# Performance work log

Hardware: AMD Instinct MI355X
Metric: run time of the kernel (lower is better)

Reference implementation:

```python
import jax, jax.numpy as jnp
import numpy as np

D_MODEL = 1024; D_STATE = 64; D_CONV = 4; EXPAND = 2; HEADDIM = 128; NGROUPS = 1; CHUNK = 256
D_INNER = EXPAND * D_MODEL            # 2048
NHEADS = D_INNER // HEADDIM           # 16
CONV_DIM = D_INNER + 2 * NGROUPS * D_STATE   # 2176
D_IN_PROJ = 2 * D_INNER + 2 * NGROUPS * D_STATE + NHEADS  # 4240
B = 4; G = 256; L = 2048
EPS = 1e-5


def setup_inputs() -> dict:
    key = jax.random.key(0)
    ks = jax.random.split(key, 12)
    def nrm(k, shape, s=0.02):
        return jax.random.normal(k, shape, jnp.float32) * s
    return dict(
        local_repr=jax.random.normal(ks[0], (B, L, D_MODEL), jnp.float32),
        global_repr=jax.random.normal(ks[1], (B, G, D_MODEL), jnp.float32),
        norm1_w=jnp.ones((D_MODEL,), jnp.float32), norm1_b=jnp.zeros((D_MODEL,), jnp.float32),
        norm2_w=jnp.ones((D_MODEL,), jnp.float32), norm2_b=jnp.zeros((D_MODEL,), jnp.float32),
        norm3_w=jnp.ones((D_MODEL,), jnp.float32), norm3_b=jnp.zeros((D_MODEL,), jnp.float32),
        in_proj_w=nrm(ks[2], (D_IN_PROJ, D_MODEL)),
        conv_w=nrm(ks[3], (CONV_DIM, D_CONV), 0.2),
        conv_b=jnp.zeros((CONV_DIM,), jnp.float32),
        dt_bias=jnp.log(jnp.expm1(jax.random.uniform(ks[4], (NHEADS,), jnp.float32, 1e-3, 0.1))),
        A_log=jnp.log(jax.random.uniform(ks[5], (NHEADS,), jnp.float32, 1.0, 16.0)),
        D_skip=jnp.ones((NHEADS,), jnp.float32),
        ssd_norm_w=jnp.ones((D_INNER,), jnp.float32),
        out_proj_w=nrm(ks[6], (D_MODEL, D_INNER)),
        ffn_w1=nrm(ks[7], (D_MODEL // 2, D_MODEL)),
        ffn_b1=jnp.zeros((D_MODEL // 2,), jnp.float32),
        ffn_w2=nrm(ks[8], (D_MODEL, D_MODEL // 2)),
        ffn_b2=jnp.zeros((D_MODEL,), jnp.float32),
    )


def _ln(x, w, b):
    mu = jnp.mean(x, axis=-1, keepdims=True)
    var = jnp.mean((x - mu) ** 2, axis=-1, keepdims=True)
    return (x - mu) * jax.lax.rsqrt(var + EPS) * w + b


def _segsum(a):
    # a: (..., T) -> (..., T, T) lower-triangular sums a[j+1..i]
    T = a.shape[-1]
    cs = jnp.cumsum(a, axis=-1)
    diff = cs[..., :, None] - cs[..., None, :]
    mask = jnp.tril(jnp.ones((T, T), bool))
    return jnp.where(mask, diff, -jnp.inf)


def _ssd(xdt, a_dt, Bh, Ch):
    # xdt: (b,t,h,p) = x*dt ; a_dt: (b,t,h) = dt*A ; Bh,Ch: (b,t,h,n)
    b, t, h, p = xdt.shape
    n = Bh.shape[-1]
    c = t // CHUNK
    X = xdt.reshape(b, c, CHUNK, h, p)
    Bc = Bh.reshape(b, c, CHUNK, h, n)
    Cc = Ch.reshape(b, c, CHUNK, h, n)
    Ac = a_dt.reshape(b, c, CHUNK, h).transpose(0, 3, 1, 2)  # (b,h,c,k)
    A_cum = jnp.cumsum(Ac, axis=-1)
    Lm = jnp.exp(_segsum(Ac))                                # (b,h,c,k,k)
    Y_diag = jnp.einsum('bckhn,bcshn,bhcks,bcshp->bckhp', Cc, Bc, Lm, X)
    decay_states = jnp.exp(A_cum[..., -1:] - A_cum)          # (b,h,c,k)
    states = jnp.einsum('bckhn,bhck,bckhp->bchpn', Bc, decay_states, X)
    A_last = jnp.pad(A_cum[..., -1], ((0, 0), (0, 0), (1, 0)))
    decay_chunk = jnp.exp(_segsum(A_last))                   # (b,h,c+1,c+1)
    states = jnp.concatenate([jnp.zeros_like(states[:, :1]), states], axis=1)
    new_states = jnp.einsum('bhzc,bchpn->bzhpn', decay_chunk, states)
    states_in = new_states[:, :-1]                           # (b,c,h,p,n)
    out_decay = jnp.exp(A_cum)                               # (b,h,c,k)
    Y_off = jnp.einsum('bckhn,bchpn,bhck->bckhp', Cc, states_in, out_decay)
    return (Y_diag + Y_off).reshape(b, t, h, p)


def _mamba2(x, in_proj_w, conv_w, conv_b, dt_bias, A_log, D_skip, ssd_norm_w, out_proj_w):
    b, t, _ = x.shape
    zxbcdt = x @ in_proj_w.T                                  # (b,t,D_IN_PROJ)
    z = zxbcdt[..., :D_INNER]
    xBC = zxbcdt[..., D_INNER:D_INNER + CONV_DIM]
    dt = jax.nn.softplus(zxbcdt[..., D_INNER + CONV_DIM:] + dt_bias)  # (b,t,h)
    # causal depthwise conv1d, kernel D_CONV
    xp = jnp.pad(xBC, ((0, 0), (D_CONV - 1, 0), (0, 0)))
    xBC = sum(xp[:, i:i + t, :] * conv_w[:, i] for i in range(D_CONV)) + conv_b
    xBC = jax.nn.silu(xBC)
    xs = xBC[..., :D_INNER].reshape(b, t, NHEADS, HEADDIM)
    Bm = xBC[..., D_INNER:D_INNER + NGROUPS * D_STATE].reshape(b, t, NGROUPS, D_STATE)
    Cm = xBC[..., D_INNER + NGROUPS * D_STATE:].reshape(b, t, NGROUPS, D_STATE)
    rep = NHEADS // NGROUPS
    Bh = jnp.repeat(Bm, rep, axis=2)
    Ch = jnp.repeat(Cm, rep, axis=2)
    A = -jnp.exp(A_log)                                       # (h,)
    Y = _ssd(xs * dt[..., None], dt * A, Bh, Ch)
    y = Y + D_skip[None, None, :, None] * xs
    y = y.reshape(b, t, D_INNER)
    # gated RMSNorm (norm_before_gate=False)
    y = y * jax.nn.silu(z)
    y = y * jax.lax.rsqrt(jnp.mean(y * y, axis=-1, keepdims=True) + EPS) * ssd_norm_w
    return y @ out_proj_w.T


def reference(local_repr, global_repr, norm1_w, norm1_b, norm2_w, norm2_b, norm3_w, norm3_b,
              in_proj_w, conv_w, conv_b, dt_bias, A_log, D_skip, ssd_norm_w, out_proj_w,
              ffn_w1, ffn_b1, ffn_w2, ffn_b2):
    local_n = _ln(local_repr, norm1_w, norm1_b)
    global_n = _ln(global_repr, norm2_w, norm2_b)
    x = jnp.concatenate([global_n, local_n], axis=1)          # (B, G+L, D)
    x = _mamba2(x, in_proj_w, conv_w, conv_b, dt_bias, A_log, D_skip, ssd_norm_w, out_proj_w)
    x = x[:, -local_n.shape[1]:, :] + local_n
    x = _ln(x, norm3_w, norm3_b)
    h = jax.nn.gelu(x @ ffn_w1.T + ffn_b1, approximate=False)
    return (h @ ffn_w2.T + ffn_b2) + x
```

## Files before the change

kernel.cpp:

```cpp
#include <hip/hip_runtime.h>
#include <math.h>

#define B_ 4
#define L_ 2048
#define G_ 256
#define T_ 2304
#define DM 1024
#define DINNER 2048
#define NH 16
#define HD 128
#define NSTATE 64
#define CONVD 2176
#define DPROJ 4240
#define NPROJ_PAD 4352
#define NCHUNK 9
#define CK 256
#define EPSV 1e-5f
#define CROWS 16

typedef unsigned short bf16t;
using bf16x8 = __attribute__((ext_vector_type(8))) short;
using f32x4  = __attribute__((ext_vector_type(4))) float;

__device__ __forceinline__ float bf2f(bf16t u) {
  return __uint_as_float(((unsigned int)u) << 16);
}
__device__ __forceinline__ bf16t f2bf(float f) {
  unsigned int u = __float_as_uint(f);
  u += 0x7FFFu + ((u >> 16) & 1u);
  return (bf16t)(u >> 16);
}

__device__ __forceinline__ void g2lds16(const bf16t* g, short* l) {
  __builtin_amdgcn_global_load_lds(
      (const __attribute__((address_space(1))) unsigned int*)g,
      (__attribute__((address_space(3))) unsigned int*)l, 16, 0, 0);
}

__device__ __forceinline__ float2 block_reduce2(float a, float b) {
  __shared__ float sa[4], sb[4];
  #pragma unroll
  for (int off = 32; off > 0; off >>= 1) {
    a += __shfl_down(a, off, 64);
    b += __shfl_down(b, off, 64);
  }
  int lane = threadIdx.x & 63, wid = threadIdx.x >> 6;
  if (lane == 0) { sa[wid] = a; sb[wid] = b; }
  __syncthreads();
  return make_float2(sa[0] + sa[1] + sa[2] + sa[3], sb[0] + sb[1] + sb[2] + sb[3]);
}

__global__ __launch_bounds__(256) void ln_cvt_kernel(
    const float* __restrict__ localr, const float* __restrict__ globalr,
    const float* __restrict__ w1, const float* __restrict__ b1,
    const float* __restrict__ w2, const float* __restrict__ b2,
    bf16t* __restrict__ x, const float* __restrict__ inpw,
    bf16t* __restrict__ inpw_bf) {
  int blk = blockIdx.x;
  if (blk < B_ * T_) {
    int t = blk % T_, b = blk / T_;
    const float *src, *w, *bb;
    if (t < G_) { src = globalr + ((long)b * G_ + t) * DM;        w = w2; bb = b2; }
    else        { src = localr  + ((long)b * L_ + (t - G_)) * DM; w = w1; bb = b1; }
    int d = threadIdx.x * 4;
    float4 v = *(const float4*)&src[d];
    float s = v.x + v.y + v.z + v.w;
    float sq = v.x * v.x + v.y * v.y + v.z * v.z + v.w * v.w;
    float2 r2 = block_reduce2(s, sq);
    float mu = r2.x * (1.f / DM);
    float var = r2.y * (1.f / DM) - mu * mu;
    float rstd = rsqrtf(var + EPSV);
    float4 wv = *(const float4*)&w[d];
    float4 bv = *(const float4*)&bb[d];
    ushort4 o;
    o.x = f2bf((v.x - mu) * rstd * wv.x + bv.x);
    o.y = f2bf((v.y - mu) * rstd * wv.y + bv.y);
    o.z = f2bf((v.z - mu) * rstd * wv.z + bv.z);
    o.w = f2bf((v.w - mu) * rstd * wv.w + bv.w);
    *(ushort4*)&x[(long)blk * DM + d] = o;
  } else {
    long i = (long)(blk - B_ * T_) * 1024 + threadIdx.x * 4;
    const long nreal = (long)DPROJ * DM, ntot = (long)NPROJ_PAD * DM;
    if (i < ntot) {
      ushort4 o = {0, 0, 0, 0};
      if (i < nreal) {
        float4 v = *(const float4*)&inpw[i];
        o.x = f2bf(v.x); o.y = f2bf(v.y); o.z = f2bf(v.z); o.w = f2bf(v.w);
      }
      *(ushort4*)&inpw_bf[i] = o;
    }
  }
}

__global__ __launch_bounds__(512, 2) void gemm_inproj(
    const bf16t* __restrict__ A, const bf16t* __restrict__ W,
    bf16t* __restrict__ z, bf16t* __restrict__ xpre, float* __restrict__ dtr) {
  __shared__ short LDS8[65536];
  int tid = threadIdx.x;
  int lane = tid & 63, w = tid >> 6;
  int wm = w >> 2, wn = w & 3;
  int l15 = lane & 15;
  int bn = blockIdx.x * 256, bm = blockIdx.y * 256;

  int csub = ((lane & 7) ^ (lane >> 3)) * 8;
  const bf16t* srcA = A + (long)(bm + w * 16 + (lane >> 3)) * 1024 + csub;
  const bf16t* srcW = W + (long)(bn + w * 16 + (lane >> 3)) * 1024 + csub;
  int stageDst = w * 1024 + lane * 8;

  int aoff0 = l15 * 64 + (((lane >> 4) + 0) ^ (lane & 7)) * 8;
  int aoff1 = l15 * 64 + (((lane >> 4) + 4) ^ (lane & 7)) * 8;
  int boff0 = ((wn & 1) * 64 + l15) * 64 + (((lane >> 4) + 0) ^ (lane & 7)) * 8;
  int boff1 = ((wn & 1) * 64 + l15) * 64 + (((lane >> 4) + 4) ^ (lane & 7)) * 8;
  int aBase0 = wm * 8192;
  int bBase0 = 16384 + (wn >> 1) * 8192;

  f32x4 acc[8][4] = {};
  bf16x8 af[4][2], bq[4][2];

#define STAGE2(gsrc, ldsoff) do { \
    g2lds16((gsrc), LDS8 + (ldsoff) + stageDst); \
    g2lds16((gsrc) + 8 * 1024, LDS8 + (ldsoff) + stageDst + 512); } while (0)

  STAGE2(srcA, 0);
  STAGE2(srcA + 128 * 1024, 8192);
  STAGE2(srcW, 16384);
  STAGE2(srcW + 128 * 1024, 24576);
  STAGE2(srcW + 64, 32768 + 16384);
  STAGE2(srcW + 128 * 1024 + 64, 32768 + 24576);
  asm volatile("s_waitcnt vmcnt(4)" ::: "memory");
  __builtin_amdgcn_s_barrier();

  const int nt = 16;
  #pragma unroll 2
  for (int t = 0; t < nt; ++t) {
    int cs_ = (t & 1) * 32768;
    int ns_ = 32768 - cs_;
    const short* aB = LDS8 + cs_ + aBase0;
    const short* bB = LDS8 + cs_ + bBase0;

    #pragma unroll
    for (int mi = 0; mi < 4; mi++) {
      af[mi][0] = *(const bf16x8*)&aB[mi * 1024 + aoff0];
      af[mi][1] = *(const bf16x8*)&aB[mi * 1024 + aoff1];
    }
    #pragma unroll
    for (int ni = 0; ni < 2; ni++) {
      bq[ni][0] = *(const bf16x8*)&bB[ni * 1024 + boff0];
      bq[ni][1] = *(const bf16x8*)&bB[ni * 1024 + boff1];
    }
    if (t + 1 < nt) STAGE2(srcA + (t + 1) * 64, ns_);
    __builtin_amdgcn_s_barrier();
    __builtin_amdgcn_s_setprio(1);
    #pragma unroll
    for (int ks = 0; ks < 2; ks++)
      #pragma unroll
      for (int mi = 0; mi < 4; mi++)
        #pragma unroll
        for (int ni = 0; ni < 2; ni++)
          acc[mi][ni] = __builtin_amdgcn_mfma_f32_16x16x32_bf16(af[mi][ks], bq[ni][ks], acc[mi][ni], 0, 0, 0);
    __builtin_amdgcn_s_setprio(0);
    __builtin_amdgcn_s_barrier();

    #pragma unroll
    for (int ni = 2; ni < 4; ni++) {
      bq[ni][0] = *(const bf16x8*)&bB[ni * 1024 + boff0];
      bq[ni][1] = *(const bf16x8*)&bB[ni * 1024 + boff1];
    }
    if (t + 1 < nt) STAGE2(srcA + 128 * 1024 + (t + 1) * 64, ns_ + 8192);
    __builtin_amdgcn_s_barrier();
    __builtin_amdgcn_s_setprio(1);
    #pragma unroll
    for (int ks = 0; ks < 2; ks++)
      #pragma unroll
      for (int mi = 0; mi < 4; mi++)
        #pragma unroll
        for (int ni = 2; ni < 4; ni++)
          acc[mi][ni] = __builtin_amdgcn_mfma_f32_16x16x32_bf16(af[mi][ks], bq[ni][ks], acc[mi][ni], 0, 0, 0);
    __builtin_amdgcn_s_setprio(0);
    __builtin_amdgcn_s_barrier();

    #pragma unroll
    for (int mi = 0; mi < 4; mi++) {
      af[mi][0] = *(const bf16x8*)&aB[(mi + 4) * 1024 + aoff0];
      af[mi][1] = *(const bf16x8*)&aB[(mi + 4) * 1024 + aoff1];
    }
    if (t + 2 < nt) STAGE2(srcW + (t + 2) * 64, cs_ + 16384);
    __builtin_amdgcn_s_barrier();
    __builtin_amdgcn_s_setprio(1);
    #pragma unroll
    for (int ks = 0; ks < 2; ks++)
      #pragma unroll
      for (int mi = 0; mi < 4; mi++)
        #pragma unroll
        for (int ni = 2; ni < 4; ni++)
          acc[mi + 4][ni] = __builtin_amdgcn_mfma_f32_16x16x32_bf16(af[mi][ks], bq[ni][ks], acc[mi + 4][ni], 0, 0, 0);
    __builtin_amdgcn_s_setprio(0);
    __builtin_amdgcn_s_barrier();

    if (t + 2 < nt) STAGE2(srcW + 128 * 1024 + (t + 2) * 64, cs_ + 24576);
    __builtin_amdgcn_s_barrier();
    __builtin_amdgcn_s_setprio(1);
    #pragma unroll
    for (int ks = 0; ks < 2; ks++)
      #pragma unroll
      for (int mi = 0; mi < 4; mi++)
        #pragma unroll
        for (int ni = 0; ni < 2; ni++)
          acc[mi + 4][ni] = __builtin_amdgcn_mfma_f32_16x16x32_bf16(af[mi][ks], bq[ni][ks], acc[mi + 4][ni], 0, 0, 0);
    __builtin_amdgcn_s_setprio(0);
    if (t + 2 < nt)      asm volatile("s_waitcnt vmcnt(4)" ::: "memory");
    else if (t + 1 < nt) asm volatile("s_waitcnt vmcnt(0)" ::: "memory");
    __builtin_amdgcn_s_barrier();
  }
#undef STAGE2

  if (bn == 4096 && wn == 2) {
    #pragma unroll
    for (int mi = 0; mi < 8; mi++)
      #pragma unroll
      for (int r = 0; r < 4; r++) {
        int row = bm + wm * 128 + mi * 16 + (lane >> 4) * 4 + r;
        dtr[(long)row * NH + l15] = acc[mi][0][r];
      }
  }

  bf16t* Cs = (bf16t*)LDS8;
  #pragma unroll
  for (int pass = 0; pass < 2; pass++) {
    __syncthreads();
    if (wm == pass) {
      #pragma unroll
      for (int mi = 0; mi < 8; mi++)
        #pragma unroll
        for (int ni = 0; ni < 4; ni++)
          #pragma unroll
          for (int r = 0; r < 4; r++)
            Cs[(mi * 16 + (lane >> 4) * 4 + r) * 264 + wn * 64 + ni * 16 + l15] =
                f2bf(acc[mi][ni][r]);
    }
    __syncthreads();
    #pragma unroll
    for (int q = 0; q < 8; q++) {
      int idx = q * 512 + tid;
      int row = idx >> 5, cg = idx & 31;
      int gcol = bn + cg * 8;
      long grow = bm + pass * 128 + row;
      if (gcol < DINNER + CONVD) {
        bf16x8 v = *(bf16x8*)&Cs[row * 264 + cg * 8];
        if (gcol < DINNER) *(bf16x8*)&z[grow * DINNER + gcol] = v;
        else               *(bf16x8*)&xpre[grow * CONVD + (gcol - DINNER)] = v;
      }
    }
  }
}

template<int EPI, bool OFFS>
__global__ __launch_bounds__(256) void gemm_mfma(
    const bf16t* __restrict__ A, const bf16t* __restrict__ W,
    const float* __restrict__ bias, const bf16t* __restrict__ res,
    float* __restrict__ Cf, bf16t* __restrict__ Cb,
    bf16t* __restrict__ z, bf16t* __restrict__ xpre, float* __restrict__ dtr,
    int N, int K) {
  __shared__ __align__(16) short LDS[128 * 136];
  short* As = LDS;
  short* Ws = LDS + 128 * 32;
  int tid = threadIdx.x;
  int lane = tid & 63, w = tid >> 6;
  int wr = w >> 1, wc = w & 1;
  int bm = blockIdx.y * 128, bn = blockIdx.x * 128;
  long bmA = OFFS ? ((long)(bm >> 11) * T_ + G_ + (bm & 2047)) : (long)bm;

  int r1 = tid >> 2,         s1 = (((tid & 3) ^ ((r1 >> 1) & 3))) * 8;
  int r2 = (tid + 256) >> 2, s2 = (((tid & 3) ^ ((r2 >> 1) & 3))) * 8;
  const bf16t* gA1 = A + (bmA + r1) * K + s1;
  const bf16t* gA2 = A + (bmA + r2) * K + s2;
  const bf16t* gW1 = W + (long)(bn + r1) * K + s1;
  const bf16t* gW2 = W + (long)(bn + r2) * K + s2;
  short* lA1 = As + tid * 8;
  short* lA2 = As + (tid + 256) * 8;
  short* lW1 = Ws + tid * 8;
  short* lW2 = Ws + (tid + 256) * 8;

  int arow = wr * 64 + (lane & 15);
  int brow = wc * 64 + (lane & 15);
  int koff = (((lane >> 4) ^ (((lane & 15) >> 1) & 3))) * 8;

  f32x4 acc[4][4] = {};
  for (int k0 = 0; k0 < K; k0 += 32) {
    g2lds16(gA1 + k0, lA1);
    g2lds16(gA2 + k0, lA2);
    g2lds16(gW1 + k0, lW1);
    g2lds16(gW2 + k0, lW2);
    __syncthreads();
    bf16x8 af[4], bf[4];
    #pragma unroll
    for (int mi = 0; mi < 4; mi++) af[mi] = *(bf16x8*)&As[(arow + mi * 16) * 32 + koff];
    #pragma unroll
    for (int ni = 0; ni < 4; ni++) bf[ni] = *(bf16x8*)&Ws[(brow + ni * 16) * 32 + koff];
    #pragma unroll
    for (int mi = 0; mi < 4; mi++)
      #pragma unroll
      for (int ni = 0; ni < 4; ni++)
        acc[mi][ni] = __builtin_amdgcn_mfma_f32_16x16x32_bf16(af[mi], bf[ni], acc[mi][ni], 0, 0, 0);
    __syncthreads();
  }

  int rb = wr * 64 + (lane >> 4) * 4;
  int cb = wc * 64 + (lane & 15);

  if (EPI == 3) {
    float* Cs32 = (float*)LDS;
    #pragma unroll
    for (int pass = 0; pass < 2; pass++) {
      __syncthreads();
      if (wr == pass) {
        #pragma unroll
        for (int mi = 0; mi < 4; mi++)
          #pragma unroll
          for (int ni = 0; ni < 4; ni++)
            #pragma unroll
            for (int r = 0; r < 4; r++) {
              int lrow = (lane >> 4) * 4 + mi * 16 + r;
              Cs32[lrow * 136 + cb + ni * 16] = acc[mi][ni][r];
            }
      }
      __syncthreads();
      #pragma unroll
      for (int q = 0; q < 4; q++) {
        int row = q * 16 + (tid >> 4);
        int col = (tid & 15) * 8;
        long grow = bm + pass * 64 + row; int gcol = bn + col;
        float4 v0 = *(float4*)&Cs32[row * 136 + col];
        float4 v1 = *(float4*)&Cs32[row * 136 + col + 4];
        float4 b0 = *(const float4*)&bias[gcol];
        float4 b1 = *(const float4*)&bias[gcol + 4];
        bf16x8 rv = *(const bf16x8*)&res[grow * N + gcol];
        v0.x += b0.x + bf2f((bf16t)rv[0]); v0.y += b0.y + bf2f((bf16t)rv[1]);
        v0.z += b0.z + bf2f((bf16t)rv[2]); v0.w += b0.w + bf2f((bf16t)rv[3]);
        v1.x += b1.x + bf2f((bf16t)rv[4]); v1.y += b1.y + bf2f((bf16t)rv[5]);
        v1.z += b1.z + bf2f((bf16t)rv[6]); v1.w += b1.w + bf2f((bf16t)rv[7]);
        *(float4*)&Cf[grow * N + gcol] = v0;
        *(float4*)&Cf[grow * N + gcol + 4] = v1;
      }
    }
    return;
  }

  __syncthreads();
  bf16t* Cs = (bf16t*)LDS;
  #pragma unroll
  for (int mi = 0; mi < 4; mi++)
    #pragma unroll
    for (int ni = 0; ni < 4; ni++)
      #pragma unroll
      for (int r = 0; r < 4; r++) {
        float v = acc[mi][ni][r];
        if (EPI == 2) {
          v += bias[bn + cb + ni * 16];
          v = 0.5f * v * (1.f + erff(v * 0.70710678118f));
        }
        Cs[(rb + mi * 16 + r) * 136 + cb + ni * 16] = f2bf(v);
      }
  __syncthreads();
  #pragma unroll
  for (int pass = 0; pass < 8; pass++) {
    int row = pass * 16 + (tid >> 4);
    int col = (tid & 15) * 8;
    bf16x8 vv = *(bf16x8*)&Cs[row * 136 + col];
    long grow = bm + row; int gcol = bn + col;
    *(bf16x8*)&Cb[grow * N + gcol] = vv;
  }
}

__global__ __launch_bounds__(256) void cumsum_kernel(
    const float* __restrict__ dtraw, const float* __restrict__ dt_bias,
    const float* __restrict__ A_log, float* __restrict__ dt,
    float* __restrict__ Acum) {
  int bid = blockIdx.x;
  int c = bid % NCHUNK; int hh = bid / NCHUNK;
  int h = hh % NH; int b = hh / NH;
  int k = threadIdx.x;
  float a = -__expf(A_log[h]);
  long t = (long)b * T_ + c * CK + k;
  float v0 = dtraw[t * NH + h] + dt_bias[h];
  float dtv = (v0 > 20.f) ? v0 : log1pf(__expf(v0));
  dt[t * NH + h] = dtv;
  float v = dtv * a;
  __shared__ float buf[2][CK];
  int cur = 0;
  buf[0][k] = v; __syncthreads();
  for (int off = 1; off < CK; off <<= 1) {
    float tv = buf[cur][k];
    if (k >= off) tv += buf[cur][k - off];
    buf[1 - cur][k] = tv; cur ^= 1; __syncthreads();
  }
  Acum[(long)bid * CK + k] = buf[cur][k];
}

__global__ __launch_bounds__(256) void conv_kernel(
    const bf16t* __restrict__ xpre, const float* __restrict__ cw,
    const float* __restrict__ cb, bf16t* __restrict__ out) {
  int gt = blockIdx.x * 256 + threadIdx.x;
  int cg = gt % 272; int rt = gt / 272;
  int c0 = cg * 8;
  long r0 = (long)rt * CROWS;
  int t0 = (int)(r0 % T_);

  float wreg[4][8];
  #pragma unroll
  for (int j = 0; j < 8; j++) {
    float4 wa = *(const float4*)&cw[(c0 + j) * 4];
    wreg[0][j] = wa.x; wreg[1][j] = wa.y; wreg[2][j] = wa.z; wreg[3][j] = wa.w;
  }
  float4 cb0 = *(const float4*)&cb[c0];
  float4 cb1 = *(const float4*)&cb[c0 + 4];
  float bias[8] = {cb0.x, cb0.y, cb0.z, cb0.w, cb1.x, cb1.y, cb1.z, cb1.w};

  bf16x8 win[4];
  #pragma unroll
  for (int i = 0; i < 3; i++) {
    if (t0 - 3 + i >= 0) win[i] = *(const bf16x8*)&xpre[(r0 - 3 + i) * CONVD + c0];
    else                 win[i] = bf16x8{0,0,0,0,0,0,0,0};
  }

  #pragma unroll
  for (int k = 0; k < CROWS; k++) {
    win[3] = *(const bf16x8*)&xpre[(r0 + k) * CONVD + c0];
    float acc[8];
    #pragma unroll
    for (int j = 0; j < 8; j++) acc[j] = bias[j];
    #pragma unroll
    for (int i = 0; i < 4; i++)
      #pragma unroll
      for (int j = 0; j < 8; j++)
        acc[j] += bf2f((bf16t)win[i][j]) * wreg[i][j];
    bf16x8 o;
    #pragma unroll
    for (int j = 0; j < 8; j++) {
      float s = acc[j] / (1.f + __expf(-acc[j]));
      o[j] = (short)f2bf(s);
    }
    *(bf16x8*)&out[(r0 + k) * CONVD + c0] = o;
    win[0] = win[1]; win[1] = win[2]; win[2] = win[3];
  }
}

__global__ __launch_bounds__(256) void chunk_states_kernel(
    const bf16t* __restrict__ xbc, const float* __restrict__ dt,
    const float* __restrict__ Acum, float* __restrict__ cs) {
  int bid = blockIdx.x;
  int h = bid & 15; int bc = bid >> 4;
  int c = bc & 7; int b = bc >> 3;
  int tid = threadIdx.x;
  int lane = tid & 63, w = tid >> 6;
  long tch = (long)b * T_ + c * CK;
  int acb = ((b * NH + h) * NCHUNK + c) * CK;
  float Alast = Acum[acb + CK - 1];

  __shared__ bf16t Xt[128][72];
  __shared__ bf16t Bt[64][72];
  __shared__ float wk[64];

  f32x4 acc[8] = {};
  for (int kb = 0; kb < 4; kb++) {
    int s0 = kb * 64;
    __syncthreads();
    if (tid < 64)
      wk[tid] = __expf(Alast - Acum[acb + s0 + tid]) * dt[(tch + s0 + tid) * NH + h];
    __syncthreads();
    for (int e = tid; e < 64 * 32; e += 256) {
      int s = e & 63, p4 = e >> 6;
      ushort4 u = *(const ushort4*)&xbc[(tch + s0 + s) * CONVD + h * HD + p4 * 4];
      float wv = wk[s];
      Xt[p4 * 4 + 0][s] = f2bf(bf2f(u.x) * wv);
      Xt[p4 * 4 + 1][s] = f2bf(bf2f(u.y) * wv);
      Xt[p4 * 4 + 2][s] = f2bf(bf2f(u.z) * wv);
      Xt[p4 * 4 + 3][s] = f2bf(bf2f(u.w) * wv);
    }
    for (int e = tid; e < 64 * 16; e += 256) {
      int s = e & 63, n4 = e >> 6;
      ushort4 u = *(const ushort4*)&xbc[(tch + s0 + s) * CONVD + DINNER + n4 * 4];
      Bt[n4 * 4 + 0][s] = u.x; Bt[n4 * 4 + 1][s] = u.y;
      Bt[n4 * 4 + 2][s] = u.z; Bt[n4 * 4 + 3][s] = u.w;
    }
    __syncthreads();
    #pragma unroll
    for (int ks = 0; ks < 2; ks++) {
      int koff = (lane >> 4) * 8 + ks * 32;
      bf16x8 bfr = *(bf16x8*)&Bt[w * 16 + (lane & 15)][koff];
      #pragma unroll
      for (int mi = 0; mi < 8; mi++) {
        bf16x8 af = *(bf16x8*)&Xt[mi * 16 + (lane & 15)][koff];
        acc[mi] = __builtin_amdgcn_mfma_f32_16x16x32_bf16(af, bfr, acc[mi], 0, 0, 0);
      }
    }
  }
  int cbid = (b * NCHUNK + c) * NH + h;
  float* out = cs + (long)cbid * HD * NSTATE;
  int n = w * 16 + (lane & 15);
  #pragma unroll
  for (int mi = 0; mi < 8; mi++) {
    #pragma unroll
    for (int r = 0; r < 4; r++) {
      int p = mi * 16 + (lane >> 4) * 4 + r;
      out[p * NSTATE + n] = acc[mi][r];
    }
  }
}

__global__ __launch_bounds__(256) void state_pass_kernel(
    float* __restrict__ cs, const float* __restrict__ Acum) {
  int bh = blockIdx.x;
  int b = bh / NH, h = bh % NH;
  int e0 = blockIdx.y * 1024 + threadIdx.x;
  for (int q = 0; q < 4; q++) {
    int e = e0 + q * 256;
    float s = 0.f;
    for (int c = 0; c < NCHUNK; c++) {
      long idx = ((long)(b * NCHUNK + c) * NH + h) * (HD * NSTATE) + e;
      if (c < NCHUNK - 1) {
        float tmp = cs[idx];
        cs[idx] = s;
        float g = __expf(Acum[((b * NH + h) * NCHUNK + c) * CK + CK - 1]);
        s = s * g + tmp;
      } else {
        cs[idx] = s;
      }
    }
  }
}

__global__ __launch_bounds__(256) void ssd_y_kernel(
    const bf16t* __restrict__ xbc, const float* __restrict__ dt,
    const float* __restrict__ Acum, const float* __restrict__ sin_,
    const float* __restrict__ Dskip, bf16t* __restrict__ Y) {
  int bid = blockIdx.x;
  int h = bid & 15; int bc = bid >> 4;
  int c = 1 + (bc & 7); int b = bc >> 3;
  int rt = blockIdx.y;
  int tid = threadIdx.x;
  int lane = tid & 63, w = tid >> 6;
  int wr = w >> 1, wc = w & 1;
  long tch = (long)b * T_ + c * CK;
  long tbase = tch + rt * 128;
  int acb = ((b * NH + h) * NCHUNK + c) * CK;

  __shared__ bf16t Cs[128][72];
  __shared__ bf16t Bs[64][72];
  __shared__ bf16t Xt[128][72];
  __shared__ bf16t Sm[128][72];
  __shared__ float Akl[128];
  __shared__ float Asl[64];
  __shared__ float dts[64];

  for (int e = tid; e < 128 * 8; e += 256) {
    int row = e >> 3, seg = (e & 7) * 8;
    *(bf16x8*)&Cs[row][seg] =
        *(const bf16x8*)&xbc[(tbase + row) * CONVD + DINNER + NSTATE + seg];
  }
  if (tid < 128) Akl[tid] = Acum[acb + rt * 128 + tid];

  f32x4 acc[4][4] = {};
  int nsb = 2 * (rt + 1);
  for (int sb = 0; sb < nsb; sb++) {
    int s0 = sb * 64;
    __syncthreads();
    if (tid < 64) {
      Asl[tid] = Acum[acb + s0 + tid];
      dts[tid] = dt[(tch + s0 + tid) * NH + h];
    }
    __syncthreads();
    for (int e = tid; e < 64 * 8; e += 256) {
      int row = e >> 3, seg = (e & 7) * 8;
      *(bf16x8*)&Bs[row][seg] =
          *(const bf16x8*)&xbc[(tch + s0 + row) * CONVD + DINNER + seg];
    }
    for (int e = tid; e < 64 * 32; e += 256) {
      int s = e & 63, p4 = e >> 6;
      ushort4 u = *(const ushort4*)&xbc[(tch + s0 + s) * CONVD + h * HD + p4 * 4];
      float dtv = dts[s];
      Xt[p4 * 4 + 0][s] = f2bf(bf2f(u.x) * dtv);
      Xt[p4 * 4 + 1][s] = f2bf(bf2f(u.y) * dtv);
      Xt[p4 * 4 + 2][s] = f2bf(bf2f(u.z) * dtv);
      Xt[p4 * 4 + 3][s] = f2bf(bf2f(u.w) * dtv);
    }
    __syncthreads();
    {
      f32x4 sacc[2][4] = {};
      int rw0 = w * 32;
      #pragma unroll
      for (int ks = 0; ks < 2; ks++) {
        int koff = (lane >> 4) * 8 + ks * 32;
        bf16x8 a0 = *(bf16x8*)&Cs[rw0 + (lane & 15)][koff];
        bf16x8 a1 = *(bf16x8*)&Cs[rw0 + 16 + (lane & 15)][koff];
        #pragma unroll
        for (int ni = 0; ni < 4; ni++) {
          bf16x8 bfr = *(bf16x8*)&Bs[ni * 16 + (lane & 15)][koff];
          sacc[0][ni] = __builtin_amdgcn_mfma_f32_16x16x32_bf16(a0, bfr, sacc[0][ni], 0, 0, 0);
          sacc[1][ni] = __builtin_amdgcn_mfma_f32_16x16x32_bf16(a1, bfr, sacc[1][ni], 0, 0, 0);
        }
      }
      #pragma unroll
      for (int mi = 0; mi < 2; mi++) {
        #pragma unroll
        for (int ni = 0; ni < 4; ni++) {
          #pragma unroll
          for (int r = 0; r < 4; r++) {
            int row = rw0 + mi * 16 + (lane >> 4) * 4 + r;
            int scol = ni * 16 + (lane & 15);
            int kglob = rt * 128 + row;
            int sglob = s0 + scol;
            float val = 0.f;
            if (sglob <= kglob) val = sacc[mi][ni][r] * __expf(Akl[row] - Asl[scol]);
            Sm[row][scol] = f2bf(val);
          }
        }
      }
    }
    __syncthreads();
    #pragma unroll
    for (int ks = 0; ks < 2; ks++) {
      int koff = (lane >> 4) * 8 + ks * 32;
      bf16x8 af[4], bfr[4];
      #pragma unroll
      for (int mi = 0; mi < 4; mi++) af[mi] = *(bf16x8*)&Sm[wr * 64 + mi * 16 + (lane & 15)][koff];
      #pragma unroll
      for (int ni = 0; ni < 4; ni++) bfr[ni] = *(bf16x8*)&Xt[wc * 64 + ni * 16 + (lane & 15)][koff];
      #pragma unroll
      for (int mi = 0; mi < 4; mi++)
        #pragma unroll
        for (int ni = 0; ni < 4; ni++)
          acc[mi][ni] = __builtin_amdgcn_mfma_f32_16x16x32_bf16(af[mi], bfr[ni], acc[mi][ni], 0, 0, 0);
    }
  }

  float ekr[16];
  #pragma unroll
  for (int mi = 0; mi < 4; mi++)
    #pragma unroll
    for (int r = 0; r < 4; r++)
      ekr[mi * 4 + r] = __expf(Akl[wr * 64 + mi * 16 + (lane >> 4) * 4 + r]);

  int cbid = (b * NCHUNK + c) * NH + h;
  const float* sinb = sin_ + (long)cbid * HD * NSTATE;
  #pragma unroll
  for (int ni = 0; ni < 4; ni++) {
    f32x4 offacc[4] = {};
    int p = wc * 64 + ni * 16 + (lane & 15);
    #pragma unroll
    for (int ks = 0; ks < 2; ks++) {
      int koff = (lane >> 4) * 8 + ks * 32;
      const float* srow = sinb + p * NSTATE + koff;
      float4 sa = *(const float4*)srow;
      float4 sbv = *(const float4*)(srow + 4);
      bf16x8 bfr;
      bfr[0] = (short)f2bf(sa.x);  bfr[1] = (short)f2bf(sa.y);
      bfr[2] = (short)f2bf(sa.z);  bfr[3] = (short)f2bf(sa.w);
      bfr[4] = (short)f2bf(sbv.x); bfr[5] = (short)f2bf(sbv.y);
      bfr[6] = (short)f2bf(sbv.z); bfr[7] = (short)f2bf(sbv.w);
      #pragma unroll
      for (int mi = 0; mi < 4; mi++) {
        bf16x8 af = *(bf16x8*)&Cs[wr * 64 + mi * 16 + (lane & 15)][koff];
        offacc[mi] = __builtin_amdgcn_mfma_f32_16x16x32_bf16(af, bfr, offacc[mi], 0, 0, 0);
      }
    }
    #pragma unroll
    for (int mi = 0; mi < 4; mi++)
      #pragma unroll
      for (int r = 0; r < 4; r++)
        acc[mi][ni][r] += ekr[mi * 4 + r] * offacc[mi][r];
  }

  float dsk = Dskip[h];
  #pragma unroll
  for (int mi = 0; mi < 4; mi++) {
    #pragma unroll
    for (int r = 0; r < 4; r++) {
      int row = wr * 64 + mi * 16 + (lane >> 4) * 4 + r;
      long t = tbase + row;
      #pragma unroll
      for (int ni = 0; ni < 4; ni++) {
        int p = wc * 64 + ni * 16 + (lane & 15);
        float xsv = bf2f(xbc[t * CONVD + h * HD + p]);
        Y[t * DINNER + h * HD + p] = f2bf(acc[mi][ni][r] + dsk * xsv);
      }
    }
  }
}

__global__ __launch_bounds__(256) void gate_rms_cvt_kernel(
    const bf16t* __restrict__ z, const float* __restrict__ nw,
    bf16t* __restrict__ Y,
    const float* __restrict__ outw, const float* __restrict__ f1w,
    const float* __restrict__ f2w, bf16t* __restrict__ o_out,
    bf16t* __restrict__ o_f1, bf16t* __restrict__ o_f2) {
  int blk = blockIdx.x;
  if (blk < B_ * L_) {
    long r = (long)(blk >> 11) * T_ + G_ + (blk & 2047);
    const bf16t* zrow = z + r * DINNER;
    bf16t* yrow = Y + r * DINNER;
    int tid = threadIdx.x;
    float v[8]; float sq = 0.f;
    #pragma unroll
    for (int i = 0; i < 4; i++) {
      int d = tid * 2 + 512 * i;
      ushort2 zu = *(const ushort2*)&zrow[d];
      ushort2 yu = *(const ushort2*)&yrow[d];
      float z0 = bf2f(zu.x), z1 = bf2f(zu.y);
      float y0 = bf2f(yu.x) * (z0 / (1.f + __expf(-z0)));
      float y1 = bf2f(yu.y) * (z1 / (1.f + __expf(-z1)));
      v[2 * i] = y0; v[2 * i + 1] = y1;
      sq += y0 * y0 + y1 * y1;
    }
    float2 r2 = block_reduce2(sq, 0.f);
    float rms = rsqrtf(r2.x * (1.f / DINNER) + EPSV);
    #pragma unroll
    for (int i = 0; i < 4; i++) {
      int d = tid * 2 + 512 * i;
      ushort2 o;
      o.x = f2bf(v[2 * i] * rms * nw[d]);
      o.y = f2bf(v[2 * i + 1] * rms * nw[d + 1]);
      *(ushort2*)&yrow[d] = o;
    }
  } else {
    long i = (long)(blk - B_ * L_) * 1024 + threadIdx.x * 4;
    const long n1 = (long)DM * DINNER;
    const long n2 = (long)(DM / 2) * DM;
    const float* src; bf16t* dst; long off;
    if (i < n1) { src = outw; dst = o_out; off = i; }
    else if (i < n1 + n2) { src = f1w; dst = o_f1; off = i - n1; }
    else { src = f2w; dst = o_f2; off = i - n1 - n2; }
    float4 v = *(const float4*)&src[off];
    ushort4 o;
    o.x = f2bf(v.x); o.y = f2bf(v.y); o.z = f2bf(v.z); o.w = f2bf(v.w);
    *(ushort4*)&dst[off] = o;
  }
}

__global__ __launch_bounds__(256) void res_ln3_kernel(
    const bf16t* __restrict__ mfull, const bf16t* __restrict__ x,
    const float* __restrict__ w3, const float* __restrict__ b3,
    bf16t* __restrict__ x2) {
  int rl = blockIdx.x;
  int tl = rl & 2047, b = rl >> 11;
  long rt = (long)b * T_ + G_ + tl;
  const bf16t* m = mfull + (long)rl * DM;
  const bf16t* xr = x + rt * DM;
  int tid = threadIdx.x;
  float v[4]; float s = 0.f, sq = 0.f;
  #pragma unroll
  for (int i = 0; i < 2; i++) {
    int d = tid * 2 + 512 * i;
    ushort2 mu2 = *(const ushort2*)&m[d];
    ushort2 xu2 = *(const ushort2*)&xr[d];
    float a0 = bf2f(mu2.x) + bf2f(xu2.x);
    float a1 = bf2f(mu2.y) + bf2f(xu2.y);
    v[2 * i] = a0; v[2 * i + 1] = a1;
    s += a0 + a1; sq += a0 * a0 + a1 * a1;
  }
  float2 r2 = block_reduce2(s, sq);
  float mu = r2.x * (1.f / DM);
  float var = r2.y * (1.f / DM) - mu * mu;
  float rstd = rsqrtf(var + EPSV);
  bf16t* dst = x2 + (long)rl * DM;
  #pragma unroll
  for (int i = 0; i < 2; i++) {
    int d = tid * 2 + 512 * i;
    ushort2 o;
    o.x = f2bf((v[2 * i] - mu) * rstd * w3[d] + b3[d]);
    o.y = f2bf((v[2 * i + 1] - mu) * rstd * w3[d + 1] + b3[d + 1]);
    *(ushort2*)&dst[d] = o;
  }
}

extern "C" void kernel_launch(void* const* d_in, const int* in_sizes, int n_in,
                              void* d_out, int out_size, void* d_ws, size_t ws_size,
                              hipStream_t stream) {
  const float* localr = (const float*)d_in[0];
  const float* globalr= (const float*)d_in[1];
  const float* n1w = (const float*)d_in[2];
  const float* n1b = (const float*)d_in[3];
  const float* n2w = (const float*)d_in[4];
  const float* n2b = (const float*)d_in[5];
  const float* n3w = (const float*)d_in[6];
  const float* n3b = (const float*)d_in[7];
  const float* inpw= (const float*)d_in[8];
  const float* convw=(const float*)d_in[9];
  const float* convb=(const float*)d_in[10];
  const float* dtb = (const float*)d_in[11];
  const float* alog= (const float*)d_in[12];
  const float* dskp= (const float*)d_in[13];
  const float* ssdw= (const float*)d_in[14];
  const float* outw= (const float*)d_in[15];
  const float* f1w = (const float*)d_in[16];
  const float* f1b = (const float*)d_in[17];
  const float* f2w = (const float*)d_in[18];
  const float* f2b = (const float*)d_in[19];

  char* ws = (char*)d_ws;
  bf16t* x     = (bf16t*)(ws + 0);
  bf16t* z     = (bf16t*)(ws + 18874368);
  bf16t* mfull = (bf16t*)(ws + 18874368);
  bf16t* xpre  = (bf16t*)(ws + 56623104);
  bf16t* Yb    = (bf16t*)(ws + 56623104);
  float* dtraw = (float*)(ws + 96731136);
  float* dt    = (float*)(ws + 97320960);
  float* Acum  = (float*)(ws + 97910784);
  bf16t* xbc   = (bf16t*)(ws + 98500608);
  bf16t* x2bf  = (bf16t*)(ws + 98500608);
  bf16t* hbuf  = (bf16t*)(ws + 115277824);
  bf16t* outw_bf = (bf16t*)(ws + 123666432);
  bf16t* f1w_bf  = (bf16t*)(ws + 127860736);
  bf16t* f2w_bf  = (bf16t*)(ws + 128909312);
  float* cs    = (float*)(ws + 138608640);
  bf16t* inpw_bf = (bf16t*)(ws + 138608640);

  ln_cvt_kernel<<<B_ * T_ + 4352, 256, 0, stream>>>(
      localr, globalr, n1w, n1b, n2w, n2b, x, inpw, inpw_bf);

  gemm_inproj<<<dim3(NPROJ_PAD / 256, (B_ * T_) / 256), 512, 0, stream>>>(
      x, inpw_bf, z, xpre, dtraw);

  cumsum_kernel<<<B_ * NH * NCHUNK, 256, 0, stream>>>(dtraw, dtb, alog, dt, Acum);

  conv_kernel<<<(B_ * T_ / CROWS) * 272 / 256, 256, 0, stream>>>(xpre, convw, convb, xbc);

  chunk_states_kernel<<<B_ * (NCHUNK - 1) * NH, 256, 0, stream>>>(xbc, dt, Acum, cs);

  state_pass_kernel<<<dim3(B_ * NH, 8), 256, 0, stream>>>(cs, Acum);

  ssd_y_kernel<<<dim3(B_ * (NCHUNK - 1) * NH, 2), 256, 0, stream>>>(
      xbc, dt, Acum, cs, dskp, Yb);

  gate_rms_cvt_kernel<<<B_ * L_ + 3072, 256, 0, stream>>>(
      z, ssdw, Yb, outw, f1w, f2w, outw_bf, f1w_bf, f2w_bf);

  gemm_mfma<1, true><<<dim3(DM / 128, (B_ * L_) / 128), 256, 0, stream>>>(
      Yb, outw_bf, nullptr, nullptr, nullptr, mfull, nullptr, nullptr, nullptr,
      DM, DINNER);

  res_ln3_kernel<<<B_ * L_, 256, 0, stream>>>(mfull, x, n3w, n3b, x2bf);

  gemm_mfma<2, false><<<dim3((DM / 2) / 128, (B_ * L_) / 128), 256, 0, stream>>>(
      x2bf, f1w_bf, f1b, nullptr, nullptr, hbuf, nullptr, nullptr, nullptr,
      DM / 2, DM);

  gemm_mfma<3, false><<<dim3(DM / 128, (B_ * L_) / 128), 256, 0, stream>>>(
      hbuf, f2w_bf, f2b, x2bf, (float*)d_out, nullptr, nullptr, nullptr, nullptr,
      DM, DM / 2);
}
```

Baseline: 501.3 us.

## Generalize in-proj GEMM to 256x128 tiles and reuse it for out-proj

```diff
diff --git a/kernel.cpp b/kernel.cpp
--- a/kernel.cpp
+++ b/kernel.cpp
@@ -92,61 +92,58 @@
   }
 }
 
-__global__ __launch_bounds__(512, 2) void gemm_inproj(
+template<int EPI, bool OFFS, int K>
+__global__ __launch_bounds__(512, 2) void gemm_wide(
     const bf16t* __restrict__ A, const bf16t* __restrict__ W,
-    bf16t* __restrict__ z, bf16t* __restrict__ xpre, float* __restrict__ dtr) {
-  __shared__ short LDS8[65536];
+    bf16t* __restrict__ Cb, bf16t* __restrict__ z, bf16t* __restrict__ xpre,
+    float* __restrict__ dtr, int N) {
+  __shared__ short LDS8[49152];
   int tid = threadIdx.x;
   int lane = tid & 63, w = tid >> 6;
-  int wm = w >> 2, wn = w & 3;
+  int wm = w >> 1, wn = w & 1;
   int l15 = lane & 15;
-  int bn = blockIdx.x * 256, bm = blockIdx.y * 256;
+  int bn = blockIdx.x * 128, bm = blockIdx.y * 256;
+  long bmA = OFFS ? ((long)(bm >> 11) * T_ + G_ + (bm & 2047)) : (long)bm;
 
   int csub = ((lane & 7) ^ (lane >> 3)) * 8;
-  const bf16t* srcA = A + (long)(bm + w * 16 + (lane >> 3)) * 1024 + csub;
-  const bf16t* srcW = W + (long)(bn + w * 16 + (lane >> 3)) * 1024 + csub;
+  const bf16t* srcA = A + (bmA + w * 16 + (lane >> 3)) * (long)K + csub;
+  const bf16t* srcW = W + (long)(bn + w * 16 + (lane >> 3)) * K + csub;
   int stageDst = w * 1024 + lane * 8;
 
-  int aoff0 = l15 * 64 + (((lane >> 4) + 0) ^ (lane & 7)) * 8;
-  int aoff1 = l15 * 64 + (((lane >> 4) + 4) ^ (lane & 7)) * 8;
-  int boff0 = ((wn & 1) * 64 + l15) * 64 + (((lane >> 4) + 0) ^ (lane & 7)) * 8;
-  int boff1 = ((wn & 1) * 64 + l15) * 64 + (((lane >> 4) + 4) ^ (lane & 7)) * 8;
-  int aBase0 = wm * 8192;
-  int bBase0 = 16384 + (wn >> 1) * 8192;
-
-  f32x4 acc[8][4] = {};
-  bf16x8 af[4][2], bq[4][2];
+  int off0 = l15 * 64 + (((lane >> 4) + 0) ^ (lane & 7)) * 8;
+  int off1 = l15 * 64 + (((lane >> 4) + 4) ^ (lane & 7)) * 8;
+
+  f32x4 acc[4][4] = {};
+  bf16x8 af[2][2], bq[4][2];
 
 #define STAGE2(gsrc, ldsoff) do { \
     g2lds16((gsrc), LDS8 + (ldsoff) + stageDst); \
-    g2lds16((gsrc) + 8 * 1024, LDS8 + (ldsoff) + stageDst + 512); } while (0)
+    g2lds16((gsrc) + 8 * (long)K, LDS8 + (ldsoff) + stageDst + 512); } while (0)
 
   STAGE2(srcA, 0);
-  STAGE2(srcA + 128 * 1024, 8192);
+  STAGE2(srcA + 128 * (long)K, 8192);
   STAGE2(srcW, 16384);
-  STAGE2(srcW + 128 * 1024, 24576);
-  STAGE2(srcW + 64, 32768 + 16384);
-  STAGE2(srcW + 128 * 1024 + 64, 32768 + 24576);
-  asm volatile("s_waitcnt vmcnt(4)" ::: "memory");
+  STAGE2(srcW + 64, 24576 + 16384);
+  asm volatile("s_waitcnt vmcnt(2)" ::: "memory");
   __builtin_amdgcn_s_barrier();
 
-  const int nt = 16;
+  const int nt = K >> 6;
   #pragma unroll 2
   for (int t = 0; t < nt; ++t) {
-    int cs_ = (t & 1) * 32768;
-    int ns_ = 32768 - cs_;
-    const short* aB = LDS8 + cs_ + aBase0;
-    const short* bB = LDS8 + cs_ + bBase0;
-
-    #pragma unroll
-    for (int mi = 0; mi < 4; mi++) {
-      af[mi][0] = *(const bf16x8*)&aB[mi * 1024 + aoff0];
-      af[mi][1] = *(const bf16x8*)&aB[mi * 1024 + aoff1];
+    int cs_ = (t & 1) * 24576;
+    int ns_ = 24576 - cs_;
+    const short* aB = LDS8 + cs_ + wm * 4096;
+    const short* bB = LDS8 + cs_ + 16384 + wn * 4096;
+
+    #pragma unroll
+    for (int mi = 0; mi < 2; mi++) {
+      af[mi][0] = *(const bf16x8*)&aB[mi * 1024 + off0];
+      af[mi][1] = *(const bf16x8*)&aB[mi * 1024 + off1];
     }
     #pragma unroll
     for (int ni = 0; ni < 2; ni++) {
-      bq[ni][0] = *(const bf16x8*)&bB[ni * 1024 + boff0];
-      bq[ni][1] = *(const bf16x8*)&bB[ni * 1024 + boff1];
+      bq[ni][0] = *(const bf16x8*)&bB[ni * 1024 + off0];
+      bq[ni][1] = *(const bf16x8*)&bB[ni * 1024 + off1];
     }
     if (t + 1 < nt) STAGE2(srcA + (t + 1) * 64, ns_);
     __builtin_amdgcn_s_barrier();
@@ -154,7 +151,7 @@
     #pragma unroll
     for (int ks = 0; ks < 2; ks++)
       #pragma unroll
-      for (int mi = 0; mi < 4; mi++)
+      for (int mi = 0; mi < 2; mi++)
         #pragma unroll
         for (int ni = 0; ni < 2; ni++)
           acc[mi][ni] = __builtin_amdgcn_mfma_f32_16x16x32_bf16(af[mi][ks], bq[ni][ks], acc[mi][ni], 0, 0, 0);
@@ -163,16 +160,16 @@
 
     #pragma unroll
     for (int ni = 2; ni < 4; ni++) {
-      bq[ni][0] = *(const bf16x8*)&bB[ni * 1024 + boff0];
-      bq[ni][1] = *(const bf16x8*)&bB[ni * 1024 + boff1];
-    }
-    if (t + 1 < nt) STAGE2(srcA + 128 * 1024 + (t + 1) * 64, ns_ + 8192);
+      bq[ni][0] = *(const bf16x8*)&bB[ni * 1024 + off0];
+      bq[ni][1] = *(const bf16x8*)&bB[ni * 1024 + off1];
+    }
+    if (t + 1 < nt) STAGE2(srcA + 128 * (long)K + (t + 1) * 64, ns_ + 8192);
     __builtin_amdgcn_s_barrier();
     __builtin_amdgcn_s_setprio(1);
     #pragma unroll
     for (int ks = 0; ks < 2; ks++)
       #pragma unroll
-      for (int mi = 0; mi < 4; mi++)
+      for (int mi = 0; mi < 2; mi++)
         #pragma unroll
         for (int ni = 2; ni < 4; ni++)
           acc[mi][ni] = __builtin_amdgcn_mfma_f32_16x16x32_bf16(af[mi][ks], bq[ni][ks], acc[mi][ni], 0, 0, 0);
@@ -180,9 +177,9 @@
     __builtin_amdgcn_s_barrier();
 
     #pragma unroll
-    for (int mi = 0; mi < 4; mi++) {
-      af[mi][0] = *(const bf16x8*)&aB[(mi + 4) * 1024 + aoff0];
-      af[mi][1] = *(const bf16x8*)&aB[(mi + 4) * 1024 + aoff1];
+    for (int mi = 0; mi < 2; mi++) {
+      af[mi][0] = *(const bf16x8*)&aB[(mi + 2) * 1024 + off0];
+      af[mi][1] = *(const bf16x8*)&aB[(mi + 2) * 1024 + off1];
     }
     if (t + 2 < nt) STAGE2(srcW + (t + 2) * 64, cs_ + 16384);
     __builtin_amdgcn_s_barrier();
@@ -190,76 +187,67 @@
     #pragma unroll
     for (int ks = 0; ks < 2; ks++)
       #pragma unroll
+      for (int mi = 0; mi < 2; mi++)
+        #pragma unroll
+        for (int ni = 0; ni < 4; ni++)
+          acc[mi + 2][ni] = __builtin_amdgcn_mfma_f32_16x16x32_bf16(af[mi][ks], bq[ni][ks], acc[mi + 2][ni], 0, 0, 0);
+    __builtin_amdgcn_s_setprio(0);
+    if (t + 2 < nt)      asm volatile("s_waitcnt vmcnt(2)" ::: "memory");
+    else if (t + 1 < nt) asm volatile("s_waitcnt vmcnt(0)" ::: "memory");
+    __builtin_amdgcn_s_barrier();
+  }
+#undef STAGE2
+
+  if (EPI == 0 && bn == 4224) {
+    if (wn == 0) {
+      #pragma unroll
       for (int mi = 0; mi < 4; mi++)
         #pragma unroll
-        for (int ni = 2; ni < 4; ni++)
-          acc[mi + 4][ni] = __builtin_amdgcn_mfma_f32_16x16x32_bf16(af[mi][ks], bq[ni][ks], acc[mi + 4][ni], 0, 0, 0);
-    __builtin_amdgcn_s_setprio(0);
-    __builtin_amdgcn_s_barrier();
-
-    if (t + 2 < nt) STAGE2(srcW + 128 * 1024 + (t + 2) * 64, cs_ + 24576);
-    __builtin_amdgcn_s_barrier();
-    __builtin_amdgcn_s_setprio(1);
-    #pragma unroll
-    for (int ks = 0; ks < 2; ks++)
+        for (int r = 0; r < 4; r++) {
+          int row = bm + wm * 64 + mi * 16 + (lane >> 4) * 4 + r;
+          dtr[(long)row * NH + l15] = acc[mi][0][r];
+        }
+    }
+    return;
+  }
+
+  bf16t* Cs = (bf16t*)LDS8;
+  #pragma unroll
+  for (int pass = 0; pass < 2; pass++) {
+    __syncthreads();
+    if ((wm >> 1) == pass) {
       #pragma unroll
       for (int mi = 0; mi < 4; mi++)
-        #pragma unroll
-        for (int ni = 0; ni < 2; ni++)
-          acc[mi + 4][ni] = __builtin_amdgcn_mfma_f32_16x16x32_bf16(af[mi][ks], bq[ni][ks], acc[mi + 4][ni], 0, 0, 0);
-    __builtin_amdgcn_s_setprio(0);
-    if (t + 2 < nt)      asm volatile("s_waitcnt vmcnt(4)" ::: "memory");
-    else if (t + 1 < nt) asm volatile("s_waitcnt vmcnt(0)" ::: "memory");
-    __builtin_amdgcn_s_barrier();
-  }
-#undef STAGE2
-
-  if (bn == 4096 && wn == 2) {
-    #pragma unroll
-    for (int mi = 0; mi < 8; mi++)
-      #pragma unroll
-      for (int r = 0; r < 4; r++) {
-        int row = bm + wm * 128 + mi * 16 + (lane >> 4) * 4 + r;
-        dtr[(long)row * NH + l15] = acc[mi][0][r];
-      }
-  }
-
-  bf16t* Cs = (bf16t*)LDS8;
-  #pragma unroll
-  for (int pass = 0; pass < 2; pass++) {
-    __syncthreads();
-    if (wm == pass) {
-      #pragma unroll
-      for (int mi = 0; mi < 8; mi++)
         #pragma unroll
         for (int ni = 0; ni < 4; ni++)
           #pragma unroll
           for (int r = 0; r < 4; r++)
-            Cs[(mi * 16 + (lane >> 4) * 4 + r) * 264 + wn * 64 + ni * 16 + l15] =
+            Cs[((wm & 1) * 64 + mi * 16 + (lane >> 4) * 4 + r) * 136 + wn * 64 + ni * 16 + l15] =
                 f2bf(acc[mi][ni][r]);
     }
     __syncthreads();
     #pragma unroll
-    for (int q = 0; q < 8; q++) {
+    for (int q = 0; q < 4; q++) {
       int idx = q * 512 + tid;
-      int row = idx >> 5, cg = idx & 31;
+      int row = idx >> 4, cg = idx & 15;
       int gcol = bn + cg * 8;
       long grow = bm + pass * 128 + row;
-      if (gcol < DINNER + CONVD) {
-        bf16x8 v = *(bf16x8*)&Cs[row * 264 + cg * 8];
+      bf16x8 v = *(bf16x8*)&Cs[row * 136 + cg * 8];
+      if (EPI == 0) {
         if (gcol < DINNER) *(bf16x8*)&z[grow * DINNER + gcol] = v;
         else               *(bf16x8*)&xpre[grow * CONVD + (gcol - DINNER)] = v;
-      }
-    }
-  }
-}
-
-template<int EPI, bool OFFS>
+      } else {
+        *(bf16x8*)&Cb[grow * (long)N + gcol] = v;
+      }
+    }
+  }
+}
+
+template<int EPI>
 __global__ __launch_bounds__(256) void gemm_mfma(
     const bf16t* __restrict__ A, const bf16t* __restrict__ W,
     const float* __restrict__ bias, const bf16t* __restrict__ res,
     float* __restrict__ Cf, bf16t* __restrict__ Cb,
-    bf16t* __restrict__ z, bf16t* __restrict__ xpre, float* __restrict__ dtr,
     int N, int K) {
   __shared__ __align__(16) short LDS[128 * 136];
   short* As = LDS;
@@ -268,12 +256,11 @@
   int lane = tid & 63, w = tid >> 6;
   int wr = w >> 1, wc = w & 1;
   int bm = blockIdx.y * 128, bn = blockIdx.x * 128;
-  long bmA = OFFS ? ((long)(bm >> 11) * T_ + G_ + (bm & 2047)) : (long)bm;
 
   int r1 = tid >> 2,         s1 = (((tid & 3) ^ ((r1 >> 1) & 3))) * 8;
   int r2 = (tid + 256) >> 2, s2 = (((tid & 3) ^ ((r2 >> 1) & 3))) * 8;
-  const bf16t* gA1 = A + (bmA + r1) * K + s1;
-  const bf16t* gA2 = A + (bmA + r2) * K + s2;
+  const bf16t* gA1 = A + (long)(bm + r1) * K + s1;
+  const bf16t* gA2 = A + (long)(bm + r2) * K + s2;
   const bf16t* gW1 = W + (long)(bn + r1) * K + s1;
   const bf16t* gW2 = W + (long)(bn + r2) * K + s2;
   short* lA1 = As + tid * 8;
@@ -818,8 +805,8 @@
   ln_cvt_kernel<<<B_ * T_ + 4352, 256, 0, stream>>>(
       localr, globalr, n1w, n1b, n2w, n2b, x, inpw, inpw_bf);
 
-  gemm_inproj<<<dim3(NPROJ_PAD / 256, (B_ * T_) / 256), 512, 0, stream>>>(
-      x, inpw_bf, z, xpre, dtraw);
+  gemm_wide<0, false, 1024><<<dim3(NPROJ_PAD / 128, (B_ * T_) / 256), 512, 0, stream>>>(
+      x, inpw_bf, nullptr, z, xpre, dtraw, NPROJ_PAD);
 
   cumsum_kernel<<<B_ * NH * NCHUNK, 256, 0, stream>>>(dtraw, dtb, alog, dt, Acum);
 
@@ -835,17 +822,14 @@
   gate_rms_cvt_kernel<<<B_ * L_ + 3072, 256, 0, stream>>>(
       z, ssdw, Yb, outw, f1w, f2w, outw_bf, f1w_bf, f2w_bf);
 
-  gemm_mfma<1, true><<<dim3(DM / 128, (B_ * L_) / 128), 256, 0, stream>>>(
-      Yb, outw_bf, nullptr, nullptr, nullptr, mfull, nullptr, nullptr, nullptr,
-      DM, DINNER);
+  gemm_wide<1, true, 2048><<<dim3(DM / 128, (B_ * L_) / 256), 512, 0, stream>>>(
+      Yb, outw_bf, mfull, nullptr, nullptr, nullptr, DM);
 
   res_ln3_kernel<<<B_ * L_, 256, 0, stream>>>(mfull, x, n3w, n3b, x2bf);
 
-  gemm_mfma<2, false><<<dim3((DM / 2) / 128, (B_ * L_) / 128), 256, 0, stream>>>(
-      x2bf, f1w_bf, f1b, nullptr, nullptr, hbuf, nullptr, nullptr, nullptr,
-      DM / 2, DM);
-
-  gemm_mfma<3, false><<<dim3(DM / 128, (B_ * L_) / 128), 256, 0, stream>>>(
-      hbuf, f2w_bf, f2b, x2bf, (float*)d_out, nullptr, nullptr, nullptr, nullptr,
-      DM, DM / 2);
-}
+  gemm_mfma<2><<<dim3((DM / 2) / 128, (B_ * L_) / 128), 256, 0, stream>>>(
+      x2bf, f1w_bf, f1b, nullptr, nullptr, hbuf, DM / 2, DM);
+
+  gemm_mfma<3><<<dim3(DM / 128, (B_ * L_) / 128), 256, 0, stream>>>(
+      hbuf, f2w_bf, f2b, x2bf, (float*)d_out, nullptr, DM, DM / 2);
+}
```

Result: faster. 485.9 us (-3.1%).
